# Kernel optimization log

Hardware: AMD Instinct MI355X
Metric: run time of the kernel (lower is better)

## Reference

```python
import jax, jax.numpy as jnp
import numpy as np

B, S, L, H, VIN, VOUT = 64, 64, 64, 256, 10000, 10000


def setup_inputs() -> dict:
    key = jax.random.key(0)
    ks = jax.random.split(key, 14)
    f = lambda k, shp: jax.random.normal(k, shp, dtype=jnp.float32) * 0.05
    return {
        "X": f(ks[0], (B, S, VIN)),
        "ground_truth": jax.random.randint(ks[1], (B, L), 0, VOUT, dtype=jnp.int32),
        "enc_Wih": f(ks[2], (3 * H, VIN)),
        "enc_Whh": f(ks[3], (3 * H, H)),
        "enc_bih": f(ks[4], (3 * H,)),
        "enc_bhh": f(ks[5], (3 * H,)),
        "att_w": f(ks[6], (2 * H,)),
        "att_b": f(ks[7], ()),
        "dec_Wih": f(ks[8], (3 * H, H + VOUT)),
        "dec_Whh": f(ks[9], (3 * H, H)),
        "dec_bih": f(ks[10], (3 * H,)),
        "dec_bhh": f(ks[11], (3 * H,)),
        "out_W": f(ks[12], (VOUT, H)),
        "out_b": f(ks[13], (VOUT,)),
    }


def gru_cell(h, x, Wih, Whh, bih, bhh):
    # PyTorch GRU cell: gates ordered (r, z, n)
    gi = x @ Wih.T + bih          # [B, 3H]
    gh = h @ Whh.T + bhh          # [B, 3H]
    ir, iz, inn = jnp.split(gi, 3, axis=-1)
    hr, hz, hn = jnp.split(gh, 3, axis=-1)
    r = jax.nn.sigmoid(ir + hr)
    z = jax.nn.sigmoid(iz + hz)
    n = jnp.tanh(inn + r * hn)
    return (1.0 - z) * n + z * h


def reference(X, ground_truth, enc_Wih, enc_Whh, enc_bih, enc_bhh,
              att_w, att_b, dec_Wih, dec_Whh, dec_bih, dec_bhh, out_W, out_b):
    b = X.shape[0]
    h_dim = enc_Whh.shape[1]
    vout = out_W.shape[0]

    # ---- encoder GRU over time (time-major scan) ----
    Xs = jnp.transpose(X, (1, 0, 2))                      # [S, B, VIN]
    h0 = jnp.zeros((b, h_dim), X.dtype)

    def enc_step(h, x):
        h2 = gru_cell(h, x, enc_Wih, enc_Whh, enc_bih, enc_bhh)
        return h2, h2

    h_last, enc_h = jax.lax.scan(enc_step, h0, Xs)        # enc_h: [S, B, H]

    # additive attention: logits = relu(W_a [h_dec; enc_h] + b_a)
    w_dec, w_enc = jnp.split(att_w, 2)                    # each [H]
    enc_score = jnp.einsum('sbh,h->sb', enc_h, w_enc)     # precomputed, [S, B]

    gtT = ground_truth.T                                  # [L, B]
    prev0 = jnp.zeros((b, vout), X.dtype)                 # initial one-hot input (zeros)

    def dec_step(carry, gt_i):
        h, prev = carry
        logits = jax.nn.relu(enc_score + h @ w_dec + att_b)   # [S, B]
        wts = jax.nn.softmax(logits, axis=0)                  # softmax over enc positions
        ctx = jnp.einsum('sb,sbh->bh', wts, enc_h)            # [B, H]
        dec_in = jnp.concatenate([ctx, prev], axis=-1)        # [B, H + VOUT]
        h2 = gru_cell(h, dec_in, dec_Wih, dec_Whh, dec_bih, dec_bhh)
        logp = jax.nn.log_softmax(h2 @ out_W.T + out_b, axis=-1)  # [B, VOUT]
        onehot = jax.nn.one_hot(gt_i, vout, dtype=X.dtype)        # teacher forcing
        return (h2, onehot), logp

    _, outs = jax.lax.scan(dec_step, (h_last, prev0), gtT)    # [L, B, VOUT]
    return jnp.transpose(outs, (1, 0, 2))                     # [B, L, VOUT]
```

## Files before the change

kernel.cpp:

```cpp
#include <hip/hip_runtime.h>
#include <hip/hip_bf16.h>
#include <math.h>

#define NB 64
#define NS 64
#define NL 64
#define NH 256
#define G3 768
#define NVIN 10000
#define NVOUT 10000
#define KP2 10240
#define NOUTP 10112

typedef __attribute__((ext_vector_type(8))) short bf16x8;
typedef __attribute__((ext_vector_type(4))) float f32x4;
typedef __attribute__((ext_vector_type(4))) unsigned int u32x4;

__device__ __forceinline__ void gld_lds16(const __hip_bfloat16* g, __hip_bfloat16* l) {
  __builtin_amdgcn_global_load_lds(
      (const __attribute__((address_space(1))) unsigned int*)(const void*)g,
      (__attribute__((address_space(3))) unsigned int*)(void*)l, 16, 0, 0);
}

__device__ __forceinline__ unsigned int f2bf(float f) {
  unsigned int u = __float_as_uint(f);
  return (u + 0x7fff + ((u >> 16) & 1)) >> 16;
}

__device__ __forceinline__ float fast_tanh(float x) {
  float e = __expf(-2.f * x);
  return (1.f - e) / (1.f + e);
}

__global__ __launch_bounds__(256) void k_cvt_pad(
    const float* __restrict__ in, __hip_bfloat16* __restrict__ out,
    int in_rows, int in_cols, int out_cols, int swz) {
  int r = blockIdx.x;
  const float* src = in + (size_t)r * in_cols;
  __hip_bfloat16* dst = out + (size_t)r * out_cols;
  bool live = r < in_rows;
  int sx = swz ? ((r & 7) << 3) : 0;
  for (int c = threadIdx.x * 4; c < out_cols; c += 1024) {
    int cc = (c & ~63) | ((c & 63) ^ sx);
    __hip_bfloat16 v[4];
    if (live && cc + 3 < in_cols) {
      float4 f = *(const float4*)(src + cc);
      v[0] = __float2bfloat16(f.x); v[1] = __float2bfloat16(f.y);
      v[2] = __float2bfloat16(f.z); v[3] = __float2bfloat16(f.w);
    } else {
      v[0] = v[1] = v[2] = v[3] = __float2bfloat16(0.f);
    }
    *(ushort4*)(dst + c) = *(const ushort4*)v;
  }
}

__global__ __launch_bounds__(256) void k_wpack(
    const float* __restrict__ srcA, int strideA,
    const float* __restrict__ srcB, int strideB,
    __hip_bfloat16* __restrict__ out, int total) {
  int idx = blockIdx.x * 256 + threadIdx.x;
  if (idx >= total) return;
  int k = idx & 255, c = (idx >> 8) & 255, f = idx >> 16;
  float v = (f < 3) ? srcA[(size_t)(f * 256 + c) * strideA + k]
                    : srcB[(size_t)((f - 3) * 256 + c) * strideB + k];
  out[idx] = __float2bfloat16(v);
}

__global__ __launch_bounds__(256) void k_gemm_encS(
    const __hip_bfloat16* __restrict__ A, const __hip_bfloat16* __restrict__ B,
    float* __restrict__ P) {
  __shared__ __hip_bfloat16 As[128][64];
  __shared__ __hip_bfloat16 Bs[128][64];
  int t = threadIdx.x;
  int wid = t >> 6, lane = t & 63;
  int m0 = blockIdx.y * 128, n0 = blockIdx.x * 128;
  int wr = wid >> 1, wc = wid & 1;
  int r16 = lane & 15, hi16 = lane >> 4;
  int xr = (r16 & 7) << 4;
  f32x4 acc[4][4] = {};
  int kbeg = blockIdx.z * 2560;
  for (int ks = 0; ks < 40; ++ks) {
    int k0 = kbeg + ks * 64;
    __syncthreads();
#pragma unroll
    for (int is = 0; is < 4; ++is) {
      int off = is * 4096 + t * 16;
      int r = off >> 7, e = (off & 127) >> 1;
      gld_lds16(A + (size_t)(m0 + r) * KP2 + k0 + e, &As[r][e]);
      gld_lds16(B + (size_t)(n0 + r) * KP2 + k0 + e, &Bs[r][e]);
    }
    __syncthreads();
    const char* ab = (const char*)As;
    const char* bb = (const char*)Bs;
#pragma unroll
    for (int kk = 0; kk < 2; ++kk) {
      int ko = kk * 64 + hi16 * 16;
      bf16x8 af[4], bfr[4];
#pragma unroll
      for (int i = 0; i < 4; ++i) {
        af[i]  = *(const bf16x8*)(ab + (wr * 64 + i * 16 + r16) * 128 + (ko ^ xr));
        bfr[i] = *(const bf16x8*)(bb + (wc * 64 + i * 16 + r16) * 128 + (ko ^ xr));
      }
#pragma unroll
      for (int i = 0; i < 4; ++i)
#pragma unroll
        for (int j = 0; j < 4; ++j)
          acc[i][j] = __builtin_amdgcn_mfma_f32_16x16x32_bf16(af[i], bfr[j], acc[i][j], 0, 0, 0);
    }
  }
  float* Pz = P + (size_t)blockIdx.z * 4096 * G3;
#pragma unroll
  for (int i = 0; i < 4; ++i)
#pragma unroll
    for (int j = 0; j < 4; ++j) {
      int ccol = n0 + wc * 64 + j * 16 + r16;
#pragma unroll
      for (int q = 0; q < 4; ++q) {
        int crow = m0 + wr * 64 + i * 16 + hi16 * 4 + q;
        Pz[(size_t)crow * G3 + ccol] = acc[i][j][q];
      }
    }
}

__global__ __launch_bounds__(256) void k_reduce4(
    const float4* __restrict__ P, const float* __restrict__ bias,
    float4* __restrict__ G) {
  int idx = blockIdx.x * 256 + threadIdx.x;
  float4 a = P[idx], b = P[idx + 786432], c = P[idx + 2 * 786432],
         d = P[idx + 3 * 786432];
  float4 bs = *(const float4*)(bias + (idx % 192) * 4);
  float4 o;
  o.x = a.x + b.x + c.x + d.x + bs.x;
  o.y = a.y + b.y + c.y + d.y + bs.y;
  o.z = a.z + b.z + c.z + d.z + bs.z;
  o.w = a.w + b.w + c.w + d.w + bs.w;
  G[idx] = o;
}

__global__ __launch_bounds__(256) void k_gemm_outS(
    const __hip_bfloat16* __restrict__ A, const __hip_bfloat16* __restrict__ B,
    const float* __restrict__ bias, float* __restrict__ C) {
  __shared__ __hip_bfloat16 As[128][64];
  __shared__ __hip_bfloat16 Bs[128][64];
  int t = threadIdx.x;
  int wid = t >> 6, lane = t & 63;
  int m0 = blockIdx.y * 128, n0 = blockIdx.x * 128;
  int wr = wid >> 1, wc = wid & 1;
  int r16 = lane & 15, hi16 = lane >> 4;
  int xr = (r16 & 7) << 4;
  f32x4 acc[4][4] = {};
  for (int k0 = 0; k0 < NH; k0 += 64) {
    __syncthreads();
#pragma unroll
    for (int is = 0; is < 4; ++is) {
      int off = is * 4096 + t * 16;
      int r = off >> 7, e = (off & 127) >> 1;
      gld_lds16(A + (size_t)(m0 + r) * NH + k0 + e, &As[r][e]);
      gld_lds16(B + (size_t)(n0 + r) * NH + k0 + e, &Bs[r][e]);
    }
    __syncthreads();
    const char* ab = (const char*)As;
    const char* bb = (const char*)Bs;
#pragma unroll
    for (int kk = 0; kk < 2; ++kk) {
      int ko = kk * 64 + hi16 * 16;
      bf16x8 af[4], bfr[4];
#pragma unroll
      for (int i = 0; i < 4; ++i) {
        af[i]  = *(const bf16x8*)(ab + (wr * 64 + i * 16 + r16) * 128 + (ko ^ xr));
        bfr[i] = *(const bf16x8*)(bb + (wc * 64 + i * 16 + r16) * 128 + (ko ^ xr));
      }
#pragma unroll
      for (int i = 0; i < 4; ++i)
#pragma unroll
        for (int j = 0; j < 4; ++j)
          acc[i][j] = __builtin_amdgcn_mfma_f32_16x16x32_bf16(af[i], bfr[j], acc[i][j], 0, 0, 0);
    }
  }
#pragma unroll
  for (int i = 0; i < 4; ++i)
#pragma unroll
    for (int j = 0; j < 4; ++j) {
      int ccol = n0 + wc * 64 + j * 16 + r16;
      if (ccol < NVOUT) {
        float bs = bias[ccol];
#pragma unroll
        for (int q = 0; q < 4; ++q) {
          int crow = m0 + wr * 64 + i * 16 + hi16 * 4 + q;
          int l = crow >> 6, b = crow & 63;
          C[((size_t)b * NL + l) * NVOUT + ccol] = acc[i][j][q] + bs;
        }
      }
    }
}

__global__ __launch_bounds__(256) void k_gemm_encw(
    const __hip_bfloat16* __restrict__ A, const __hip_bfloat16* __restrict__ B,
    __hip_bfloat16* __restrict__ CT) {
  __shared__ __hip_bfloat16 As[128][32];
  __shared__ __hip_bfloat16 Bs[128][32];
  int t = threadIdx.x;
  int wid = t >> 6, lane = t & 63;
  int m0 = blockIdx.y * 128, n0 = blockIdx.x * 128;
  int wr = wid >> 1, wc = wid & 1;
  f32x4 acc[4][4] = {};
  for (int k0 = 0; k0 < NH; k0 += 32) {
    __syncthreads();
#pragma unroll
    for (int is = 0; is < 2; ++is) {
      int off = is * 4096 + wid * 1024 + lane * 16;
      int r = off >> 6, cb = (off & 63) >> 1;
      gld_lds16(A + (size_t)(m0 + r) * NH + k0 + cb, &As[r][cb]);
      gld_lds16(B + (size_t)(n0 + r) * NH + k0 + cb, &Bs[r][cb]);
    }
    __syncthreads();
    int r16 = lane & 15, kb = (lane >> 4) * 8;
    bf16x8 af[4], bfr[4];
#pragma unroll
    for (int i = 0; i < 4; ++i) {
      af[i]  = *(const bf16x8*)&As[wr * 64 + i * 16 + r16][kb];
      bfr[i] = *(const bf16x8*)&Bs[wc * 64 + i * 16 + r16][kb];
    }
#pragma unroll
    for (int i = 0; i < 4; ++i)
#pragma unroll
      for (int j = 0; j < 4; ++j)
        acc[i][j] = __builtin_amdgcn_mfma_f32_16x16x32_bf16(af[i], bfr[j], acc[i][j], 0, 0, 0);
  }
  int r16 = lane & 15, rg = lane >> 4;
#pragma unroll
  for (int i = 0; i < 4; ++i)
#pragma unroll
    for (int j = 0; j < 4; ++j) {
      int ccol = n0 + wc * 64 + j * 16 + r16;
#pragma unroll
      for (int q = 0; q < 4; ++q) {
        int crow = m0 + wr * 64 + i * 16 + rg * 4 + q;
        int bb = crow >> 6, ss = crow & 63;
        CT[((size_t)bb * G3 + ccol) * 64 + (ss ^ ((ccol & 7) << 3))] =
            __float2bfloat16(acc[i][j][q]);
      }
    }
}

__global__ __launch_bounds__(256) void k_pregather(
    const float* __restrict__ Wih, const float* __restrict__ bih,
    const int* __restrict__ gt, float* __restrict__ Gdec) {
  int ib = blockIdx.x;
  int i = ib >> 6, b = ib & 63;
  int tok = (i > 0) ? gt[b * NL + (i - 1)] : -1;
  for (int g = threadIdx.x; g < G3; g += 256) {
    float v = bih[g];
    if (tok >= 0) v += Wih[(size_t)g * (NH + NVOUT) + NH + tok];
    Gdec[(size_t)ib * G3 + g] = v;
  }
}

__global__ __launch_bounds__(512, 2) void k_encoder4(
    const float* __restrict__ Gi, const __hip_bfloat16* __restrict__ Wcat,
    const float* __restrict__ bhh, const float* __restrict__ att_w,
    __hip_bfloat16* __restrict__ enchB, float* __restrict__ escoreT) {
  __shared__ float h32[2][256];
  __shared__ __hip_bfloat16 hbf[2][256];
  int t = threadIdx.x, w = t >> 6, lane = t & 63;
  int b = blockIdx.x;
  int r16 = lane & 15, hi16 = lane >> 4;
  bf16x8 wv[3][2][8];
#pragma unroll
  for (int f = 0; f < 3; ++f)
#pragma unroll
    for (int fc = 0; fc < 2; ++fc)
#pragma unroll
      for (int kf = 0; kf < 8; ++kf)
        wv[f][fc][kf] = *(const bf16x8*)(Wcat +
            (((size_t)f * 256 + w * 32 + fc * 16 + r16) * 256 + kf * 32 + hi16 * 8));
  float aw[4];
#pragma unroll
  for (int q = 0; q < 4; ++q) aw[q] = att_w[256 + lane + q * 64];
  if (t < 256) {
    h32[0][t] = 0.f; h32[1][t] = 0.f;
    hbf[0][t] = __float2bfloat16(0.f); hbf[1][t] = __float2bfloat16(0.f);
  }
  __syncthreads();
  int cur = 0;
  for (int s = 0; s < NS; ++s) {
    float gd[3][2];
    if (hi16 == 0) {
#pragma unroll
      for (int f = 0; f < 3; ++f)
#pragma unroll
        for (int fc = 0; fc < 2; ++fc)
          gd[f][fc] = Gi[((size_t)b * 64 + s) * G3 + f * 256 + w * 32 + fc * 16 + lane];
    }
    const char* hb = (const char*)&hbf[cur][0];
    f32x4 acc[3][2] = {};
#pragma unroll
    for (int half = 0; half < 2; ++half) {
      bf16x8 ah[4];
#pragma unroll
      for (int kf = 0; kf < 4; ++kf)
        ah[kf] = *(const bf16x8*)(hb + (half * 4 + kf) * 64 + hi16 * 16);
#pragma unroll
      for (int f = 0; f < 3; ++f)
#pragma unroll
        for (int fc = 0; fc < 2; ++fc)
#pragma unroll
          for (int kf = 0; kf < 4; ++kf)
            acc[f][fc] = __builtin_amdgcn_mfma_f32_16x16x32_bf16(
                ah[kf], wv[f][fc][half * 4 + kf], acc[f][fc], 0, 0, 0);
    }
    if (hi16 == 0) {
      int nxt = cur ^ 1;
#pragma unroll
      for (int fc = 0; fc < 2; ++fc) {
        int c = w * 32 + fc * 16 + lane;
        float rr = 1.f / (1.f + __expf(-(gd[0][fc] + acc[0][fc][0] + bhh[c])));
        float zz = 1.f / (1.f + __expf(-(gd[1][fc] + acc[1][fc][0] + bhh[256 + c])));
        float nn = fast_tanh(gd[2][fc] + rr * (acc[2][fc][0] + bhh[512 + c]));
        float hn = (1.f - zz) * nn + zz * h32[cur][c];
        h32[nxt][c] = hn;
        hbf[nxt][c] = __float2bfloat16(hn);
        enchB[((size_t)b * 64 + s) * 256 + c] = __float2bfloat16(hn);
      }
    }
    __syncthreads();
    cur ^= 1;
    if (w == 0) {
      float p = h32[cur][lane] * aw[0] + h32[cur][lane + 64] * aw[1]
              + h32[cur][lane + 128] * aw[2] + h32[cur][lane + 192] * aw[3];
#pragma unroll
      for (int off = 32; off; off >>= 1) p += __shfl_xor(p, off, 64);
      if (lane == 0) escoreT[(size_t)b * 64 + s] = p;
    }
  }
}

__global__ __launch_bounds__(512, 2) void k_decoder5(
    const float* __restrict__ Gdec, const __hip_bfloat16* __restrict__ Wcat6,
    const float* __restrict__ bhh, const __hip_bfloat16* __restrict__ enchB,
    const __hip_bfloat16* __restrict__ ENCWT, const float* __restrict__ escoreT,
    const float* __restrict__ att_w, const float* __restrict__ att_b,
    __hip_bfloat16* __restrict__ dechb) {
  __shared__ __hip_bfloat16 encwT[G3][64];
  __shared__ __hip_bfloat16 hbf[2][256];
  __shared__ float h32[2][256];
  int t = threadIdx.x, w = t >> 6, lane = t & 63;
  int b = blockIdx.x;
  int r16 = lane & 15, hi16 = lane >> 4;
  int cw = w * 32;
  {
    const char* srcb = (const char*)(ENCWT + (size_t)b * G3 * 64);
    char* dstb = (char*)&encwT[0][0];
#pragma unroll
    for (int is = 0; is < 12; ++is) {
      int off = is * 8192 + t * 16;
      gld_lds16((const __hip_bfloat16*)(srcb + off), (__hip_bfloat16*)(dstb + off));
    }
  }
  bf16x8 wv[2][2][8];
#pragma unroll
  for (int f = 0; f < 2; ++f)
#pragma unroll
    for (int fc = 0; fc < 2; ++fc)
#pragma unroll
      for (int kf = 0; kf < 8; ++kf)
        wv[f][fc][kf] = *(const bf16x8*)(Wcat6 +
            (((size_t)(3 + f) * 256 + cw + fc * 16 + r16) * 256 + kf * 32 + hi16 * 8));
  float aw[4];
#pragma unroll
  for (int q = 0; q < 4; ++q) aw[q] = att_w[lane + q * 64];
  float attb = att_b[0];
  float esc = escoreT[(size_t)b * 64 + lane];
  float bh0[2], bh1[2], bh2[2];
#pragma unroll
  for (int fc = 0; fc < 2; ++fc) {
    bh0[fc] = bhh[cw + fc * 16 + r16];
    bh1[fc] = bhh[256 + cw + fc * 16 + r16];
    bh2[fc] = bhh[512 + cw + fc * 16 + r16];
  }
  if (t < 256) {
    float v = __bfloat162float(enchB[((size_t)b * 64 + 63) * 256 + t]);
    h32[0][t] = v;  hbf[0][t] = __float2bfloat16(v);
    h32[1][t] = 0.f; hbf[1][t] = __float2bfloat16(0.f);
  }
  __syncthreads();
  float hp[2];
  hp[0] = h32[0][cw + r16];
  hp[1] = h32[0][cw + 16 + r16];
  int bs3 = (b & 7) << 3;
  unsigned long long wna = (unsigned long long)(Wcat6 + (size_t)5 * 256 * 256);
  int cur = 0;
  for (int i = 0; i < NL; ++i) {
    asm volatile("" : "+v"(wna));
    const __hip_bfloat16* wnp = (const __hip_bfloat16*)wna;
    float gd0[2], gd1[2], gd2[2];
    if (hi16 == 0) {
      const float* gp = Gdec + ((size_t)i * 64 + b) * G3;
#pragma unroll
      for (int fc = 0; fc < 2; ++fc) {
        gd0[fc] = gp[cw + fc * 16 + r16];
        gd1[fc] = gp[256 + cw + fc * 16 + r16];
        gd2[fc] = gp[512 + cw + fc * 16 + r16];
      }
    }
    float p = h32[cur][lane] * aw[0] + h32[cur][lane + 64] * aw[1]
            + h32[cur][lane + 128] * aw[2] + h32[cur][lane + 192] * aw[3];
#pragma unroll
    for (int off = 32; off; off >>= 1) p += __shfl_xor(p, off, 64);
    float lg = fmaxf(esc + p + attb, 0.f);
    float mx = lg;
#pragma unroll
    for (int off = 32; off; off >>= 1) mx = fmaxf(mx, __shfl_xor(mx, off, 64));
    float e = __expf(lg - mx);
    float sm = e;
#pragma unroll
    for (int off = 32; off; off >>= 1) sm += __shfl_xor(sm, off, 64);
    float wl = e / sm;
    bf16x8 af_[2];
#pragma unroll
    for (int kf = 0; kf < 2; ++kf) {
      u32x4 tmp;
#pragma unroll
      for (int j = 0; j < 4; ++j) {
        int src = hi16 * 8 + kf * 32 + 2 * j;
        tmp[j] = f2bf(__shfl(wl, src, 64)) | (f2bf(__shfl(wl, src + 1, 64)) << 16);
      }
      af_[kf] = __builtin_bit_cast(bf16x8, tmp);
    }
    f32x4 acc_rz[2][2] = {};
    f32x4 ghn2[2] = {};
    f32x4 gin2[2] = {};
    const char* eb = (const char*)&encwT[0][0];
#pragma unroll
    for (int g = 0; g < 3; ++g)
#pragma unroll
      for (int fc = 0; fc < 2; ++fc) {
        int cloc = g * 256 + cw + fc * 16 + r16;
        int xb = (cloc & 7) << 4;
#pragma unroll
        for (int kf = 0; kf < 2; ++kf) {
          bf16x8 bfrag = *(const bf16x8*)(eb + cloc * 128 + ((kf * 64 + hi16 * 16) ^ xb));
          if (g < 2) acc_rz[g][fc] = __builtin_amdgcn_mfma_f32_16x16x32_bf16(af_[kf], bfrag, acc_rz[g][fc], 0, 0, 0);
          else       gin2[fc]     = __builtin_amdgcn_mfma_f32_16x16x32_bf16(af_[kf], bfrag, gin2[fc], 0, 0, 0);
        }
      }
    const char* hb = (const char*)&hbf[cur][0];
#pragma unroll
    for (int half = 0; half < 2; ++half) {
      bf16x8 ah[4];
#pragma unroll
      for (int kf = 0; kf < 4; ++kf)
        ah[kf] = *(const bf16x8*)(hb + (half * 4 + kf) * 64 + hi16 * 16);
      bf16x8 wn[2][4];
#pragma unroll
      for (int fc = 0; fc < 2; ++fc)
#pragma unroll
        for (int kf = 0; kf < 4; ++kf)
          wn[fc][kf] = *(const bf16x8*)(wnp +
              ((size_t)(cw + fc * 16 + r16) * 256 + (half * 4 + kf) * 32 + hi16 * 8));
#pragma unroll
      for (int f = 0; f < 2; ++f)
#pragma unroll
        for (int fc = 0; fc < 2; ++fc)
#pragma unroll
          for (int kf = 0; kf < 4; ++kf)
            acc_rz[f][fc] = __builtin_amdgcn_mfma_f32_16x16x32_bf16(
                ah[kf], wv[f][fc][half * 4 + kf], acc_rz[f][fc], 0, 0, 0);
#pragma unroll
      for (int fc = 0; fc < 2; ++fc)
#pragma unroll
        for (int kf = 0; kf < 4; ++kf)
          ghn2[fc] = __builtin_amdgcn_mfma_f32_16x16x32_bf16(
              ah[kf], wn[fc][kf], ghn2[fc], 0, 0, 0);
    }
    if (hi16 == 0) {
      int nxt = cur ^ 1;
#pragma unroll
      for (int fc = 0; fc < 2; ++fc) {
        int c = cw + fc * 16 + r16;
        float rr = 1.f / (1.f + __expf(-(gd0[fc] + acc_rz[0][fc][0] + bh0[fc])));
        float zz = 1.f / (1.f + __expf(-(gd1[fc] + acc_rz[1][fc][0] + bh1[fc])));
        float nn = fast_tanh(gd2[fc] + gin2[fc][0] + rr * (ghn2[fc][0] + bh2[fc]));
        float hn = (1.f - zz) * nn + zz * hp[fc];
        hp[fc] = hn;
        h32[nxt][c] = hn;
        hbf[nxt][c] = __float2bfloat16(hn);
        int cs = (c & ~63) | ((c & 63) ^ bs3);
        dechb[((size_t)i * 64 + b) * 256 + cs] = __float2bfloat16(hn);
      }
    }
    __syncthreads();
    cur ^= 1;
  }
}

__global__ __launch_bounds__(256) void k_logsoftmax(float* __restrict__ out) {
  float* x = out + (size_t)blockIdx.x * NVOUT;
  __shared__ float red[256];
  int t = threadIdx.x;
  float4 v[10];
  float mx = -1e30f;
#pragma unroll
  for (int ii = 0; ii < 10; ++ii) {
    int slot = ii * 256 + t;
    if (slot < 2500) {
      v[ii] = *(const float4*)(x + slot * 4);
      mx = fmaxf(mx, fmaxf(fmaxf(v[ii].x, v[ii].y), fmaxf(v[ii].z, v[ii].w)));
    }
  }
  red[t] = mx; __syncthreads();
  for (int off = 128; off; off >>= 1) {
    if (t < off) red[t] = fmaxf(red[t], red[t + off]);
    __syncthreads();
  }
  mx = red[0]; __syncthreads();
  float sm = 0.f;
#pragma unroll
  for (int ii = 0; ii < 10; ++ii) {
    int slot = ii * 256 + t;
    if (slot < 2500)
      sm += __expf(v[ii].x - mx) + __expf(v[ii].y - mx)
          + __expf(v[ii].z - mx) + __expf(v[ii].w - mx);
  }
  red[t] = sm; __syncthreads();
  for (int off = 128; off; off >>= 1) {
    if (t < off) red[t] += red[t + off];
    __syncthreads();
  }
  float lse = mx + logf(red[0]);
#pragma unroll
  for (int ii = 0; ii < 10; ++ii) {
    int slot = ii * 256 + t;
    if (slot < 2500) {
      float4 o; o.x = v[ii].x - lse; o.y = v[ii].y - lse;
      o.z = v[ii].z - lse; o.w = v[ii].w - lse;
      *(float4*)(x + slot * 4) = o;
    }
  }
}

extern "C" void kernel_launch(void* const* d_in, const int* in_sizes, int n_in,
                              void* d_out, int out_size, void* d_ws, size_t ws_size,
                              hipStream_t stream) {
  const float* X        = (const float*)d_in[0];
  const int*   gt       = (const int*)  d_in[1];
  const float* enc_Wih  = (const float*)d_in[2];
  const float* enc_Whh  = (const float*)d_in[3];
  const float* enc_bih  = (const float*)d_in[4];
  const float* enc_bhh  = (const float*)d_in[5];
  const float* att_w    = (const float*)d_in[6];
  const float* att_b    = (const float*)d_in[7];
  const float* dec_Wih  = (const float*)d_in[8];
  const float* dec_Whh  = (const float*)d_in[9];
  const float* dec_bih  = (const float*)d_in[10];
  const float* dec_bhh  = (const float*)d_in[11];
  const float* out_W    = (const float*)d_in[12];
  const float* out_b    = (const float*)d_in[13];
  float* out = (float*)d_out;

  float* p = (float*)d_ws;
  float* Gienc  = p; p += NS * NB * G3;
  float* Gdec   = p; p += NL * NB * G3;
  float* escoreT = p; p += NB * NS;
  __hip_bfloat16* q = (__hip_bfloat16*)p;
  __hip_bfloat16* enchBb = q; q += (size_t)NB * NS * NH;
  __hip_bfloat16* Wcat_e = q; q += (size_t)3 * 256 * 256;
  __hip_bfloat16* Wcat_d = q; q += (size_t)6 * 256 * 256;
  __hip_bfloat16* Xb     = q; q += (size_t)4096 * KP2;
  __hip_bfloat16* Wencb  = q; q += (size_t)G3 * KP2;
  __hip_bfloat16* Woutb  = q; q += (size_t)NOUTP * NH;
  __hip_bfloat16* dechb  = q; q += (size_t)NL * NB * NH;
  __hip_bfloat16* ENCWT  = (__hip_bfloat16*)Gienc;
  float* Pout = (float*)d_out;

  k_cvt_pad<<<4096, 256, 0, stream>>>(X, Xb, 4096, NVIN, KP2, 1);
  k_cvt_pad<<<G3, 256, 0, stream>>>(enc_Wih, Wencb, G3, NVIN, KP2, 1);
  k_cvt_pad<<<NOUTP, 256, 0, stream>>>(out_W, Woutb, NVOUT, NH, NH, 1);
  k_wpack<<<768, 256, 0, stream>>>(enc_Whh, NH, enc_Whh, NH, Wcat_e, 3 * 65536);
  k_wpack<<<1536, 256, 0, stream>>>(dec_Wih, NH + NVOUT, dec_Whh, NH, Wcat_d, 6 * 65536);
  k_pregather<<<NL * NB, 256, 0, stream>>>(dec_Wih, dec_bih, gt, Gdec);

  k_gemm_encS<<<dim3(6, 32, 4), 256, 0, stream>>>(Xb, Wencb, Pout);
  k_reduce4<<<3072, 256, 0, stream>>>((const float4*)Pout, enc_bih, (float4*)Gienc);
  k_encoder4<<<64, 512, 0, stream>>>(Gienc, Wcat_e, enc_bhh, att_w, enchBb, escoreT);
  k_gemm_encw<<<dim3(6, 32), 256, 0, stream>>>(enchBb, Wcat_d, ENCWT);
  k_decoder5<<<64, 512, 0, stream>>>(Gdec, Wcat_d, dec_bhh, enchBb, ENCWT,
                                     escoreT, att_w, att_b, dechb);
  k_gemm_outS<<<dim3(79, 32), 256, 0, stream>>>(dechb, Woutb, out_b, out);
  k_logsoftmax<<<NB * NL, 256, 0, stream>>>(out);
}
```

Measured before the change: 838.8 us.

## Keep decoder Whh in registers and defer softmax normalization into gate math

The decoder now keeps all three Whh gate slices in registers instead of reloading the n-gate slice from global memory every step, and computes the h-projection MFMAs before the attention path. The attention softmax drops the max-subtraction and the two wave reductions: it uses unnormalized exp weights, computes their sum with an MFMA against a ones vector, and scales the context projection by the reciprocal afterwards. This shortens the serial per-step dependency chain. The costs are higher register pressure (launch_bounds min-blocks removed on both recurrent kernels) and possible overflow, because exp is taken without max-subtraction, which is safe only while the relu logits stay small.

```diff
diff --git a/kernel.cpp b/kernel.cpp
--- a/kernel.cpp
+++ b/kernel.cpp
@@ -256,7 +256,7 @@
   }
 }
 
-__global__ __launch_bounds__(512, 2) void k_encoder4(
+__global__ __launch_bounds__(512) void k_encoder4(
     const float* __restrict__ Gi, const __hip_bfloat16* __restrict__ Wcat,
     const float* __restrict__ bhh, const float* __restrict__ att_w,
     __hip_bfloat16* __restrict__ enchB, float* __restrict__ escoreT) {
@@ -335,7 +335,7 @@
   }
 }
 
-__global__ __launch_bounds__(512, 2) void k_decoder5(
+__global__ __launch_bounds__(512) void k_decoder6(
     const float* __restrict__ Gdec, const __hip_bfloat16* __restrict__ Wcat6,
     const float* __restrict__ bhh, const __hip_bfloat16* __restrict__ enchB,
     const __hip_bfloat16* __restrict__ ENCWT, const float* __restrict__ escoreT,
@@ -357,9 +357,9 @@
       gld_lds16((const __hip_bfloat16*)(srcb + off), (__hip_bfloat16*)(dstb + off));
     }
   }
-  bf16x8 wv[2][2][8];
-#pragma unroll
-  for (int f = 0; f < 2; ++f)
+  bf16x8 wv[3][2][8];
+#pragma unroll
+  for (int f = 0; f < 3; ++f)
 #pragma unroll
     for (int fc = 0; fc < 2; ++fc)
 #pragma unroll
@@ -378,6 +378,8 @@
     bh1[fc] = bhh[256 + cw + fc * 16 + r16];
     bh2[fc] = bhh[512 + cw + fc * 16 + r16];
   }
+  u32x4 onesu = {0x3F803F80u, 0x3F803F80u, 0x3F803F80u, 0x3F803F80u};
+  bf16x8 onesf = __builtin_bit_cast(bf16x8, onesu);
   if (t < 256) {
     float v = __bfloat162float(enchB[((size_t)b * 64 + 63) * 256 + t]);
     h32[0][t] = v;  hbf[0][t] = __float2bfloat16(v);
@@ -388,11 +390,8 @@
   hp[0] = h32[0][cw + r16];
   hp[1] = h32[0][cw + 16 + r16];
   int bs3 = (b & 7) << 3;
-  unsigned long long wna = (unsigned long long)(Wcat6 + (size_t)5 * 256 * 256);
   int cur = 0;
   for (int i = 0; i < NL; ++i) {
-    asm volatile("" : "+v"(wna));
-    const __hip_bfloat16* wnp = (const __hip_bfloat16*)wna;
     float gd0[2], gd1[2], gd2[2];
     if (hi16 == 0) {
       const float* gp = Gdec + ((size_t)i * 64 + b) * G3;
@@ -403,19 +402,29 @@
         gd2[fc] = gp[512 + cw + fc * 16 + r16];
       }
     }
+    const char* hb = (const char*)&hbf[cur][0];
+    f32x4 acch[3][2] = {};
+#pragma unroll
+    for (int half = 0; half < 2; ++half) {
+      bf16x8 ah[4];
+#pragma unroll
+      for (int kf = 0; kf < 4; ++kf)
+        ah[kf] = *(const bf16x8*)(hb + (half * 4 + kf) * 64 + hi16 * 16);
+#pragma unroll
+      for (int f = 0; f < 3; ++f)
+#pragma unroll
+        for (int fc = 0; fc < 2; ++fc)
+#pragma unroll
+          for (int kf = 0; kf < 4; ++kf)
+            acch[f][fc] = __builtin_amdgcn_mfma_f32_16x16x32_bf16(
+                ah[kf], wv[f][fc][half * 4 + kf], acch[f][fc], 0, 0, 0);
+    }
     float p = h32[cur][lane] * aw[0] + h32[cur][lane + 64] * aw[1]
             + h32[cur][lane + 128] * aw[2] + h32[cur][lane + 192] * aw[3];
 #pragma unroll
     for (int off = 32; off; off >>= 1) p += __shfl_xor(p, off, 64);
     float lg = fmaxf(esc + p + attb, 0.f);
-    float mx = lg;
-#pragma unroll
-    for (int off = 32; off; off >>= 1) mx = fmaxf(mx, __shfl_xor(mx, off, 64));
-    float e = __expf(lg - mx);
-    float sm = e;
-#pragma unroll
-    for (int off = 32; off; off >>= 1) sm += __shfl_xor(sm, off, 64);
-    float wl = e / sm;
+    float e = __expf(lg);
     bf16x8 af_[2];
 #pragma unroll
     for (int kf = 0; kf < 2; ++kf) {
@@ -423,13 +432,14 @@
 #pragma unroll
       for (int j = 0; j < 4; ++j) {
         int src = hi16 * 8 + kf * 32 + 2 * j;
-        tmp[j] = f2bf(__shfl(wl, src, 64)) | (f2bf(__shfl(wl, src + 1, 64)) << 16);
+        tmp[j] = f2bf(__shfl(e, src, 64)) | (f2bf(__shfl(e, src + 1, 64)) << 16);
       }
       af_[kf] = __builtin_bit_cast(bf16x8, tmp);
     }
-    f32x4 acc_rz[2][2] = {};
-    f32x4 ghn2[2] = {};
-    f32x4 gin2[2] = {};
+    f32x4 smacc = {};
+    smacc = __builtin_amdgcn_mfma_f32_16x16x32_bf16(af_[0], onesf, smacc, 0, 0, 0);
+    smacc = __builtin_amdgcn_mfma_f32_16x16x32_bf16(af_[1], onesf, smacc, 0, 0, 0);
+    f32x4 acci[3][2] = {};
     const char* eb = (const char*)&encwT[0][0];
 #pragma unroll
     for (int g = 0; g < 3; ++g)
@@ -440,47 +450,19 @@
 #pragma unroll
         for (int kf = 0; kf < 2; ++kf) {
           bf16x8 bfrag = *(const bf16x8*)(eb + cloc * 128 + ((kf * 64 + hi16 * 16) ^ xb));
-          if (g < 2) acc_rz[g][fc] = __builtin_amdgcn_mfma_f32_16x16x32_bf16(af_[kf], bfrag, acc_rz[g][fc], 0, 0, 0);
-          else       gin2[fc]     = __builtin_amdgcn_mfma_f32_16x16x32_bf16(af_[kf], bfrag, gin2[fc], 0, 0, 0);
+          acci[g][fc] = __builtin_amdgcn_mfma_f32_16x16x32_bf16(
+              af_[kf], bfrag, acci[g][fc], 0, 0, 0);
         }
       }
-    const char* hb = (const char*)&hbf[cur][0];
-#pragma unroll
-    for (int half = 0; half < 2; ++half) {
-      bf16x8 ah[4];
-#pragma unroll
-      for (int kf = 0; kf < 4; ++kf)
-        ah[kf] = *(const bf16x8*)(hb + (half * 4 + kf) * 64 + hi16 * 16);
-      bf16x8 wn[2][4];
-#pragma unroll
-      for (int fc = 0; fc < 2; ++fc)
-#pragma unroll
-        for (int kf = 0; kf < 4; ++kf)
-          wn[fc][kf] = *(const bf16x8*)(wnp +
-              ((size_t)(cw + fc * 16 + r16) * 256 + (half * 4 + kf) * 32 + hi16 * 8));
-#pragma unroll
-      for (int f = 0; f < 2; ++f)
-#pragma unroll
-        for (int fc = 0; fc < 2; ++fc)
-#pragma unroll
-          for (int kf = 0; kf < 4; ++kf)
-            acc_rz[f][fc] = __builtin_amdgcn_mfma_f32_16x16x32_bf16(
-                ah[kf], wv[f][fc][half * 4 + kf], acc_rz[f][fc], 0, 0, 0);
-#pragma unroll
-      for (int fc = 0; fc < 2; ++fc)
-#pragma unroll
-        for (int kf = 0; kf < 4; ++kf)
-          ghn2[fc] = __builtin_amdgcn_mfma_f32_16x16x32_bf16(
-              ah[kf], wn[fc][kf], ghn2[fc], 0, 0, 0);
-    }
     if (hi16 == 0) {
+      float rn = 1.f / smacc[0];
       int nxt = cur ^ 1;
 #pragma unroll
       for (int fc = 0; fc < 2; ++fc) {
         int c = cw + fc * 16 + r16;
-        float rr = 1.f / (1.f + __expf(-(gd0[fc] + acc_rz[0][fc][0] + bh0[fc])));
-        float zz = 1.f / (1.f + __expf(-(gd1[fc] + acc_rz[1][fc][0] + bh1[fc])));
-        float nn = fast_tanh(gd2[fc] + gin2[fc][0] + rr * (ghn2[fc][0] + bh2[fc]));
+        float rr = 1.f / (1.f + __expf(-(gd0[fc] + acci[0][fc][0] * rn + acch[0][fc][0] + bh0[fc])));
+        float zz = 1.f / (1.f + __expf(-(gd1[fc] + acci[1][fc][0] * rn + acch[1][fc][0] + bh1[fc])));
+        float nn = fast_tanh(gd2[fc] + acci[2][fc][0] * rn + rr * (acch[2][fc][0] + bh2[fc]));
         float hn = (1.f - zz) * nn + zz * hp[fc];
         hp[fc] = hn;
         h32[nxt][c] = hn;
@@ -584,7 +566,7 @@
   k_reduce4<<<3072, 256, 0, stream>>>((const float4*)Pout, enc_bih, (float4*)Gienc);
   k_encoder4<<<64, 512, 0, stream>>>(Gienc, Wcat_e, enc_bhh, att_w, enchBb, escoreT);
   k_gemm_encw<<<dim3(6, 32), 256, 0, stream>>>(enchBb, Wcat_d, ENCWT);
-  k_decoder5<<<64, 512, 0, stream>>>(Gdec, Wcat_d, dec_bhh, enchBb, ENCWT,
+  k_decoder6<<<64, 512, 0, stream>>>(Gdec, Wcat_d, dec_bhh, enchBb, ENCWT,
                                      escoreT, att_w, att_b, dechb);
   k_gemm_outS<<<dim3(79, 32), 256, 0, stream>>>(dechb, Woutb, out_b, out);
   k_logsoftmax<<<NB * NL, 256, 0, stream>>>(out);
```

New measurement: 789.4 us. -5.9%, faster.
